# Kernel tuning notes

Measured on AMD Instinct MI355X. Metric: run time of the kernel, lower is better.

## Reference

```python
import jax, jax.numpy as jnp
import numpy as np
import math

H = 16          # n_heads
D = 1024        # hidden_dim
HD = D // H     # head_dim = 64
LR = 256        # Linformer low-rank length L
MAX_T = 4096    # max_seq_len


def setup_inputs() -> dict:
    key = jax.random.key(0)
    ks = jax.random.split(key, 7)
    X = jax.random.normal(ks[0], (4, 4096, D), dtype=jnp.float32)
    # lecun_normal ~ N(0, 1/fan_in)
    W_kernel = jax.random.normal(ks[1], (D, 3 * D), dtype=jnp.float32) / math.sqrt(D)
    W_bias = jnp.zeros((3 * D,), dtype=jnp.float32)
    low_rank_E = jax.random.normal(ks[2], (MAX_T, H, LR), dtype=jnp.float32) / math.sqrt(MAX_T)
    low_rank_V = jax.random.normal(ks[3], (MAX_T, H, LR), dtype=jnp.float32) / math.sqrt(MAX_T)
    o_kernel = jax.random.normal(ks[4], (D, D), dtype=jnp.float32) / math.sqrt(D)
    o_bias = jnp.zeros((D,), dtype=jnp.float32)
    return {"X": X, "W_kernel": W_kernel, "W_bias": W_bias,
            "low_rank_E": low_rank_E, "low_rank_V": low_rank_V,
            "o_kernel": o_kernel, "o_bias": o_bias}


def reference(X, W_kernel, W_bias, low_rank_E, low_rank_V, o_kernel, o_bias):
    B, T, _ = X.shape
    # L2-normalize tokens
    norm = jnp.linalg.norm(X, ord=2, axis=-1, keepdims=True)  # (B,T,1)
    Xn = X / norm
    # fused QKV projection
    qkv = Xn @ W_kernel + W_bias                 # (B,T,3D)
    qkv = qkv.reshape(B, T, 3, H, HD)
    Q, K, V = qkv[:, :, 0], qkv[:, :, 1], qkv[:, :, 2]   # (B,T,H,HD)
    # low-rank sequence projection of K/V: T -> L
    E = low_rank_E[:T]                            # (T,H,L)
    F = low_rank_V[:T]                            # (T,H,L)
    Kp = jnp.einsum('THK,BTHD->BHKD', E, K)       # (B,H,L,HD)
    Vp = jnp.einsum('THK,BTHD->BHKD', F, V)       # (B,H,L,HD)
    Qh = Q.transpose(0, 2, 1, 3)                  # (B,H,T,HD)
    logits = jnp.einsum('BHTD,BHKD->BHTK', Qh, Kp) / math.sqrt(HD)
    attn = jax.nn.softmax(logits, axis=-1)        # (B,H,T,L)
    out = jnp.einsum('BHTK,BHKD->BHTD', attn, Vp) # (B,H,T,HD)
    out = out.transpose(0, 2, 1, 3).reshape(B, T, H * HD)
    return out @ o_kernel + o_bias
```

## Files before the change

kernel.cpp:

```cpp
#include <hip/hip_runtime.h>
#include <stdint.h>

typedef unsigned short u16;
typedef uint32_t u32;
typedef __bf16 bf16x8 __attribute__((ext_vector_type(8)));
typedef float f32x4 __attribute__((ext_vector_type(4)));

__device__ __forceinline__ u16 f2bf(float f) {
    u32 u = __builtin_bit_cast(u32, f);
    u += 0x7fffu + ((u >> 16) & 1u);
    return (u16)(u >> 16);
}

__device__ __forceinline__ f32x4 mfma16(bf16x8 a, bf16x8 b, f32x4 c) {
    return __builtin_amdgcn_mfma_f32_16x16x32_bf16(a, b, c, 0, 0, 0);
}

__device__ __forceinline__ void gld_lds16(void* lds, const void* g) {
    __builtin_amdgcn_global_load_lds(
        (__attribute__((address_space(1))) void*)(uintptr_t)g,
        (__attribute__((address_space(3))) void*)(u32)(uintptr_t)lds,
        16, 0, 0);
}

__global__ __launch_bounds__(256) void k_norm(const float* __restrict__ X,
                                              u16* __restrict__ Xn) {
    const int row = blockIdx.x;
    const float4 v = ((const float4*)(X + (size_t)row * 1024))[threadIdx.x];
    float ss = v.x * v.x + v.y * v.y + v.z * v.z + v.w * v.w;
#pragma unroll
    for (int m = 1; m < 64; m <<= 1) ss += __shfl_xor(ss, m);
    __shared__ float red[4];
    if ((threadIdx.x & 63) == 0) red[threadIdx.x >> 6] = ss;
    __syncthreads();
    const float sc = 1.0f / sqrtf(red[0] + red[1] + red[2] + red[3]);
    ushort4 o;
    o.x = f2bf(v.x * sc); o.y = f2bf(v.y * sc);
    o.z = f2bf(v.z * sc); o.w = f2bf(v.w * sc);
    ((ushort4*)(Xn + (size_t)row * 1024))[threadIdx.x] = o;
}

__global__ __launch_bounds__(256) void k_transpose_cast64(
    const float* __restrict__ src, u16* __restrict__ dst,
    int R, int rstride, long zsrc, long zdst) {
    __shared__ float tile[64][65];
    src += (size_t)blockIdx.z * zsrc;
    dst += (size_t)blockIdx.z * zdst;
    const int c0 = blockIdx.x * 64, r0 = blockIdx.y * 64;
    const int tid = threadIdx.x;
    const int lr = tid >> 4, lc = tid & 15;
#pragma unroll
    for (int i = 0; i < 4; ++i) {
        const int r = lr + i * 16;
        const float4 v = *(const float4*)(src + (size_t)(r0 + r) * rstride + c0 + lc * 4);
        tile[r][lc * 4 + 0] = v.x; tile[r][lc * 4 + 1] = v.y;
        tile[r][lc * 4 + 2] = v.z; tile[r][lc * 4 + 3] = v.w;
    }
    __syncthreads();
    const int c = tid >> 2, seg = tid & 3;
    u32 w[8];
#pragma unroll
    for (int j = 0; j < 8; ++j) {
        const u32 lo = f2bf(tile[seg * 16 + 2 * j][c]);
        const u32 hi = f2bf(tile[seg * 16 + 2 * j + 1][c]);
        w[j] = lo | (hi << 16);
    }
    u16* dp = dst + (size_t)(c0 + c) * R + r0 + seg * 16;
    uint4 q0; q0.x = w[0]; q0.y = w[1]; q0.z = w[2]; q0.w = w[3];
    uint4 q1; q1.x = w[4]; q1.y = w[5]; q1.z = w[6]; q1.w = w[7];
    *(uint4*)dp = q0;
    *((uint4*)dp + 1) = q1;
}

#define G8_PRE(Aptr, Bptr)                                                       \
    const int tid = threadIdx.x, lane = tid & 63;                                \
    const int wid = tid >> 6, wm = wid >> 2, wn = wid & 3;                       \
    const int cl = lane & 15, g = lane >> 4;                                     \
    const int colb = (tid & 7) * 16;                                             \
    const int scb = colb ^ (((tid >> 3) & 7) << 4);                              \
    const int rbA = ((tid >> 3) & 31) + ((tid >> 8) << 7);                       \
    const int rbB = tid >> 3;                                                    \
    const char* gA = (const char*)(Aptr) + (size_t)(m0 + rbA) * 2048 + scb;      \
    const char* gB = (const char*)(Bptr) + (size_t)(n0 + rbB) * 2048 + scb;      \
    const u32 lA = (u32)(rbA * 128 + colb);                                      \
    const u32 lB = (u32)(65536 + rbB * 128 + colb);                              \
    const int xr0 = (g * 16) ^ ((cl & 7) << 4);                                  \
    const int xr1 = (64 + g * 16) ^ ((cl & 7) << 4);

#define G8_STA(q, tau, beta) gld_lds16(sm + (beta) + lA + (q) * 4096,            \
                                       gA + (q) * 65536 + (size_t)(tau) * 128);
#define G8_STB(c, tau, beta) gld_lds16(sm + (beta) + lB + (c) * 8192,            \
                                       gB + (c) * 131072 + (size_t)(tau) * 128);

#define G8_RDB(beta)                                                             \
    _Pragma("unroll") for (int nf = 0; nf < 4; ++nf) {                           \
        const u32 rb_ = (beta) + 65536 + (u32)(wn * 64 + nf * 16 + cl) * 128;    \
        bF[nf][0] = *(const bf16x8*)(sm + rb_ + xr0);                            \
        bF[nf][1] = *(const bf16x8*)(sm + rb_ + xr1);                            \
    }
#define G8_RDA(q, beta)                                                          \
    _Pragma("unroll") for (int m = 0; m < 2; ++m) {                              \
        const u32 ra_ = (beta) + (u32)(wm * 128 + (q) * 32 + m * 16 + cl) * 128; \
        aF[m][0] = *(const bf16x8*)(sm + ra_ + xr0);                             \
        aF[m][1] = *(const bf16x8*)(sm + ra_ + xr1);                             \
    }

#define G8_MMA(q)                                                                \
    asm volatile("s_waitcnt lgkmcnt(0)" ::: "memory");                           \
    __builtin_amdgcn_sched_barrier(0);                                           \
    __builtin_amdgcn_s_setprio(1);                                               \
    _Pragma("unroll") for (int m = 0; m < 2; ++m)                                \
        _Pragma("unroll") for (int nf = 0; nf < 4; ++nf) {                       \
            acc[(q)*2 + m][nf] = mfma16(aF[m][0], bF[nf][0], acc[(q)*2 + m][nf]);\
            acc[(q)*2 + m][nf] = mfma16(aF[m][1], bF[nf][1], acc[(q)*2 + m][nf]);\
        }                                                                        \
    __builtin_amdgcn_s_setprio(0);                                               \
    __builtin_amdgcn_s_barrier();                                                \
    __builtin_amdgcn_sched_barrier(0);

#define G8_LOOP                                                                  \
    bf16x8 aF[2][2], bF[4][2];                                                   \
    G8_STA(0, 0, 0) G8_STB(0, 0, 0) G8_STA(1, 0, 0) G8_STB(1, 0, 0)              \
    G8_STA(2, 0, 0) G8_STB(2, 0, 0) G8_STA(3, 0, 0) G8_STB(3, 0, 0)              \
    G8_STA(0, 1, 32768) G8_STB(0, 1, 32768)                                      \
    G8_STA(1, 1, 32768) G8_STB(1, 1, 32768)                                      \
    G8_STA(2, 1, 32768) G8_STB(2, 1, 32768)                                      \
    for (int it = 0; it < 8; ++it) {                                             \
        const int t1 = 2 * it + 1, t2v = 2 * it + 2, t3v = 2 * it + 3;           \
        const bool nt = (it < 7);                                                \
                                                                         \
        G8_STA(3, t1, 32768) G8_STB(3, t1, 32768)                                \
        asm volatile("s_waitcnt vmcnt(8)" ::: "memory");                         \
        __builtin_amdgcn_s_barrier();                                            \
        G8_RDB(0) G8_RDA(0, 0) G8_MMA(0)                                         \
                                                                         \
        if (nt) { G8_STA(0, t2v, 0) G8_STB(0, t2v, 0) }                          \
        G8_RDA(1, 0) G8_MMA(1)                                                   \
                                                                         \
        if (nt) { G8_STA(1, t2v, 0) G8_STB(1, t2v, 0) }                          \
        G8_RDA(2, 0) G8_MMA(2)                                                   \
                                                                         \
        if (nt) { G8_STA(2, t2v, 0) G8_STB(2, t2v, 0) }                          \
        G8_RDA(3, 0) G8_MMA(3)                                                   \
                                                                         \
        if (nt) {                                                                \
            G8_STA(3, t2v, 0) G8_STB(3, t2v, 0)                                  \
            asm volatile("s_waitcnt vmcnt(8)" ::: "memory");                     \
        } else {                                                                 \
            asm volatile("s_waitcnt vmcnt(0)" ::: "memory");                     \
        }                                                                        \
        __builtin_amdgcn_s_barrier();                                            \
        G8_RDB(32768) G8_RDA(0, 32768) G8_MMA(0)                                 \
                                                                         \
        if (nt) { G8_STA(0, t3v, 32768) G8_STB(0, t3v, 32768) }                  \
        G8_RDA(1, 32768) G8_MMA(1)                                               \
                                                                         \
        if (nt) { G8_STA(1, t3v, 32768) G8_STB(1, t3v, 32768) }                  \
        G8_RDA(2, 32768) G8_MMA(2)                                               \
                                                                         \
        if (nt) { G8_STA(2, t3v, 32768) G8_STB(2, t3v, 32768) }                  \
        G8_RDA(3, 32768) G8_MMA(3)                                               \
    }

__global__ __launch_bounds__(512, 2) void k_gemm_qkv(
    const u16* __restrict__ A, const u16* __restrict__ Bt,
    const float* __restrict__ bias,
    u16* __restrict__ Qo, u16* __restrict__ Kt, u16* __restrict__ Vt) {
    __shared__ __align__(16) char sm[131072];
    u32 bid = blockIdx.x;
    bid = (bid & 7) * 96 + (bid >> 3);
    const int m0 = (int)(bid / 12) * 256, n0 = (int)(bid % 12) * 256;

    G8_PRE(A, Bt)

    const f32x4 fz = {0.f, 0.f, 0.f, 0.f};
    f32x4 acc[8][4];
#pragma unroll
    for (int i = 0; i < 8; ++i)
#pragma unroll
        for (int j = 0; j < 4; ++j) acc[i][j] = fz;

    G8_LOOP

#pragma unroll
    for (int mf = 0; mf < 8; ++mf) {
        const int mbase = m0 + wm * 128 + mf * 16 + g * 4;
        const int b = mbase >> 12;
        const int t = mbase & 4095;
#pragma unroll
        for (int nf = 0; nf < 4; ++nf) {
            const int n = n0 + wn * 64 + nf * 16 + cl;
            const float bv = bias[n];
            const int seg = n >> 10;
            const int hd = n & 1023;
            f32x4 v = acc[mf][nf];
            if (seg == 0) {
#pragma unroll
                for (int r = 0; r < 4; ++r)
                    Qo[(size_t)(mbase + r) * 1024 + hd] = f2bf(v[r] + bv);
            } else {
                u16* dst = (seg == 1) ? Kt : Vt;
                ushort4 pk;
                pk.x = f2bf(v[0] + bv); pk.y = f2bf(v[1] + bv);
                pk.z = f2bf(v[2] + bv); pk.w = f2bf(v[3] + bv);
                *(ushort4*)(dst + (size_t)(b * 1024 + hd) * 4096 + t) = pk;
            }
        }
    }
}

__global__ __launch_bounds__(512, 2) void k_gemm_out(
    const u16* __restrict__ A, const u16* __restrict__ Bt,
    const float* __restrict__ bias, float* __restrict__ out) {
    __shared__ __align__(16) char sm[131072];
    u32 bid = blockIdx.x;
    bid = (bid & 7) * 32 + (bid >> 3);
    const int m0 = (int)(bid / 4) * 256, n0 = (int)(bid % 4) * 256;

    G8_PRE(A, Bt)

    const f32x4 fz = {0.f, 0.f, 0.f, 0.f};
    f32x4 acc[8][4];
#pragma unroll
    for (int i = 0; i < 8; ++i)
#pragma unroll
        for (int j = 0; j < 4; ++j) acc[i][j] = fz;

    G8_LOOP

#pragma unroll
    for (int mf = 0; mf < 8; ++mf) {
        const int mbase = m0 + wm * 128 + mf * 16 + g * 4;
#pragma unroll
        for (int nf = 0; nf < 4; ++nf) {
            const int n = n0 + wn * 64 + nf * 16 + cl;
            const float bv = bias[n];
            f32x4 v = acc[mf][nf];
#pragma unroll
            for (int r = 0; r < 4; ++r)
                out[(size_t)(mbase + r) * 1024 + n] = v[r] + bv;
        }
    }
}

__global__ __launch_bounds__(512) void k_gemm_kpvp(
    const u16* __restrict__ Et, const u16* __restrict__ Ft,
    const u16* __restrict__ Kt, const u16* __restrict__ Vt,
    float* __restrict__ Pp) {
    __shared__ __align__(16) char sm[49152];
    const int tid = threadIdx.x, lane = tid & 63, wid = tid >> 6;
    const int wm = wid >> 2, wn = wid & 3;
    const int cl = lane & 15, g = lane >> 4;
    const int mT = blockIdx.x;
    const int hs = blockIdx.y;
    const int h = hs & 15, s = hs >> 4;
    const int ks = blockIdx.z;

    const u16* Ab = (s ? Ft : Et) + (size_t)h * (256 * 4096)
                    + (size_t)(mT * 128) * 4096 + ks * 1024;
    const u16* Bb = s ? Vt : Kt;

    const int rA = tid >> 2, c16 = tid & 3;
    const int scol = (c16 ^ ((rA >> 1) & 3)) * 8;
    const u16* gA = Ab + (size_t)rA * 4096 + scol;
    const int rB1 = rA + 128;
    const u16* gB0 = Bb + (size_t)((((rA >> 6) * 16 + h) * 64) + (rA & 63)) * 4096
                     + ks * 1024 + scol;
    const u16* gB1 = Bb + (size_t)((((rB1 >> 6) * 16 + h) * 64) + (rB1 & 63)) * 4096
                     + ks * 1024 + scol;
    const u32 lA = (u32)(rA * 64 + c16 * 16);
    const u32 lB0 = (u32)(8192 + rA * 64 + c16 * 16);
    const u32 lB1 = (u32)(8192 + rB1 * 64 + c16 * 16);
    const int xsw = (g ^ ((cl >> 1) & 3)) * 16;

    const f32x4 fz = {0.f, 0.f, 0.f, 0.f};
    f32x4 acc[4][4];
#pragma unroll
    for (int i = 0; i < 4; ++i)
#pragma unroll
        for (int j = 0; j < 4; ++j) acc[i][j] = fz;

    gld_lds16(sm + lA, gA); gld_lds16(sm + lB0, gB0); gld_lds16(sm + lB1, gB1);

    u32 roff = 0;
    for (int kt = 0; kt < 32; ++kt) {
        const u32 woff = roff ^ 24576;
        if (kt < 31) {
            gld_lds16(sm + woff + lA, gA + (kt + 1) * 32);
            gld_lds16(sm + woff + lB0, gB0 + (kt + 1) * 32);
            gld_lds16(sm + woff + lB1, gB1 + (kt + 1) * 32);
            asm volatile("s_waitcnt vmcnt(3)" ::: "memory");
        } else {
            asm volatile("s_waitcnt vmcnt(0)" ::: "memory");
        }
        __builtin_amdgcn_s_barrier();
        __builtin_amdgcn_sched_barrier(0);
        const char* rb = sm + roff;
        bf16x8 aF[4], bF[4];
#pragma unroll
        for (int mf = 0; mf < 4; ++mf)
            aF[mf] = *(const bf16x8*)(rb + (wm * 64 + mf * 16 + cl) * 64 + xsw);
#pragma unroll
        for (int nf = 0; nf < 4; ++nf)
            bF[nf] = *(const bf16x8*)(rb + 8192 + (wn * 64 + nf * 16 + cl) * 64 + xsw);
        asm volatile("s_waitcnt lgkmcnt(0)" ::: "memory");
        __builtin_amdgcn_sched_barrier(0);
        __builtin_amdgcn_s_setprio(1);
#pragma unroll
        for (int mf = 0; mf < 4; ++mf)
#pragma unroll
            for (int nf = 0; nf < 4; ++nf)
                acc[mf][nf] = mfma16(aF[mf], bF[nf], acc[mf][nf]);
        __builtin_amdgcn_s_setprio(0);
        asm volatile("s_waitcnt lgkmcnt(0)" ::: "memory");
        __builtin_amdgcn_s_barrier();
        roff = woff;
    }

    float* P = Pp + ((size_t)(ks * 32 + hs) << 16);
#pragma unroll
    for (int mf = 0; mf < 4; ++mf) {
        const int m = mT * 128 + wm * 64 + mf * 16 + g * 4;
#pragma unroll
        for (int nf = 0; nf < 4; ++nf) {
            const int dcat = wn * 64 + nf * 16 + cl;
            f32x4 v = acc[mf][nf];
#pragma unroll
            for (int r = 0; r < 4; ++r)
                P[(size_t)(m + r) * 256 + dcat] = v[r];
        }
    }
}

__global__ __launch_bounds__(256) void k_red(const float* __restrict__ Pp,
                                             u16* __restrict__ Kp,
                                             u16* __restrict__ Vpt) {
    const int e = blockIdx.x * 256 + threadIdx.x;
    const int hs = e >> 14;
    const int rem = (e & 16383) * 4;
    float4 sum = {0.f, 0.f, 0.f, 0.f};
#pragma unroll
    for (int ks = 0; ks < 4; ++ks) {
        const float4 v = *(const float4*)(Pp + (((size_t)(ks * 32 + hs)) << 16) + rem);
        sum.x += v.x; sum.y += v.y; sum.z += v.z; sum.w += v.w;
    }
    const int m = rem >> 8, dcat = rem & 255;
    const int h = hs & 15, sf = hs >> 4;
    const int bh = (dcat >> 6) * 16 + h, d0 = dcat & 63;
    if (sf == 0) {
        ushort4 pk;
        pk.x = f2bf(sum.x); pk.y = f2bf(sum.y);
        pk.z = f2bf(sum.z); pk.w = f2bf(sum.w);
        *(ushort4*)(Kp + (size_t)bh * 16384 + m * 64 + d0) = pk;
    } else {
        u16* vp = Vpt + (size_t)bh * 16384 + m;
        vp[(d0 + 0) * 256] = f2bf(sum.x);
        vp[(d0 + 1) * 256] = f2bf(sum.y);
        vp[(d0 + 2) * 256] = f2bf(sum.z);
        vp[(d0 + 3) * 256] = f2bf(sum.w);
    }
}

__global__ __launch_bounds__(256, 1) void k_attn(
    const u16* __restrict__ Q, const u16* __restrict__ Kp,
    const u16* __restrict__ Vpt, u16* __restrict__ AO) {
    __shared__ __align__(16) char sm[65536];
    const int lane = threadIdx.x & 63, wid = threadIdx.x >> 6;
    const int cl = lane & 15, g = lane >> 4;
    const int tT = blockIdx.x, h = blockIdx.y, b = blockIdx.z;
    const int bh = b * 16 + h;
    const int trow0 = b * 4096 + tT * 128 + wid * 32;
    const u16* Qb = Q + (size_t)trow0 * 1024 + h * 64;
    const u16* KpB = Kp + (size_t)bh * (256 * 64);
    const u16* VpB = Vpt + (size_t)bh * (64 * 256);
    char* sP = sm + wid * 16384;

    bf16x8 qF[2][2];
#pragma unroll
    for (int nf = 0; nf < 2; ++nf)
#pragma unroll
        for (int ks = 0; ks < 2; ++ks)
            qF[nf][ks] = *(const bf16x8*)(Qb + (size_t)(nf * 16 + cl) * 1024 + ks * 32 + g * 8);

    const f32x4 fz = {0.f, 0.f, 0.f, 0.f};
    f32x4 Sp[16][2];
#pragma unroll
    for (int mf = 0; mf < 16; ++mf) { Sp[mf][0] = fz; Sp[mf][1] = fz; }

#pragma unroll
    for (int mf = 0; mf < 16; ++mf) {
#pragma unroll
        for (int ks = 0; ks < 2; ++ks) {
            bf16x8 aF = *(const bf16x8*)(KpB + (size_t)(mf * 16 + cl) * 64 + ks * 32 + g * 8);
            Sp[mf][0] = mfma16(aF, qF[0][ks], Sp[mf][0]);
            Sp[mf][1] = mfma16(aF, qF[1][ks], Sp[mf][1]);
        }
    }

    float inv_sum[2];
#pragma unroll
    for (int nf = 0; nf < 2; ++nf) {
        float mx = -1e30f;
#pragma unroll
        for (int mf = 0; mf < 16; ++mf)
#pragma unroll
            for (int r = 0; r < 4; ++r) {
                float x = Sp[mf][nf][r] * 0.125f;
                Sp[mf][nf][r] = x;
                mx = fmaxf(mx, x);
            }
        mx = fmaxf(mx, __shfl_xor(mx, 16));
        mx = fmaxf(mx, __shfl_xor(mx, 32));
        float sum = 0.f;
#pragma unroll
        for (int mf = 0; mf < 16; ++mf)
#pragma unroll
            for (int r = 0; r < 4; ++r) {
                float p = __expf(Sp[mf][nf][r] - mx);
                Sp[mf][nf][r] = p;
                sum += p;
            }
        sum += __shfl_xor(sum, 16);
        sum += __shfl_xor(sum, 32);
        inv_sum[nf] = 1.0f / sum;

        const int tl = nf * 16 + cl;
        const int sw = (tl & 7) << 4;
#pragma unroll
        for (int mf = 0; mf < 16; ++mf) {
            uint2 pk;
            pk.x = (u32)f2bf(Sp[mf][nf][0]) | ((u32)f2bf(Sp[mf][nf][1]) << 16);
            pk.y = (u32)f2bf(Sp[mf][nf][2]) | ((u32)f2bf(Sp[mf][nf][3]) << 16);
            *(uint2*)(sP + ((tl * 512 + (mf * 16 + g * 4) * 2) ^ sw)) = pk;
        }
    }

    f32x4 Oa[4][2];
#pragma unroll
    for (int mf = 0; mf < 4; ++mf) { Oa[mf][0] = fz; Oa[mf][1] = fz; }
#pragma unroll
    for (int ks = 0; ks < 8; ++ks) {
        bf16x8 aF[4];
#pragma unroll
        for (int mf = 0; mf < 4; ++mf)
            aF[mf] = *(const bf16x8*)(VpB + (size_t)(mf * 16 + cl) * 256 + ks * 32 + g * 8);
#pragma unroll
        for (int nf = 0; nf < 2; ++nf) {
            const int tl = nf * 16 + cl;
            const int sw = (tl & 7) << 4;
            bf16x8 bF = *(const bf16x8*)(sP + ((tl * 512 + (ks * 32 + g * 8) * 2) ^ sw));
#pragma unroll
            for (int mf = 0; mf < 4; ++mf)
                Oa[mf][nf] = mfma16(aF[mf], bF, Oa[mf][nf]);
        }
    }

#pragma unroll
    for (int nf = 0; nf < 2; ++nf) {
        const int t = trow0 + nf * 16 + cl;
#pragma unroll
        for (int mf = 0; mf < 4; ++mf) {
            f32x4 v = Oa[mf][nf];
            ushort4 pk;
            pk.x = f2bf(v[0] * inv_sum[nf]); pk.y = f2bf(v[1] * inv_sum[nf]);
            pk.z = f2bf(v[2] * inv_sum[nf]); pk.w = f2bf(v[3] * inv_sum[nf]);
            *(ushort4*)(AO + (size_t)t * 1024 + h * 64 + mf * 16 + g * 4) = pk;
        }
    }
}

extern "C" void kernel_launch(void* const* d_in, const int* in_sizes, int n_in,
                              void* d_out, int out_size, void* d_ws, size_t ws_size,
                              hipStream_t stream) {
    const float* X  = (const float*)d_in[0];
    const float* Wk = (const float*)d_in[1];
    const float* Wb = (const float*)d_in[2];
    const float* E  = (const float*)d_in[3];
    const float* F  = (const float*)d_in[4];
    const float* Ok = (const float*)d_in[5];
    const float* Ob = (const float*)d_in[6];
    float* out = (float*)d_out;
    char* ws = (char*)d_ws;

    u16* Xn  = (u16*)(ws + 0);
    u16* Wt  = (u16*)(ws + 33554432);
    u16* Ot  = (u16*)(ws + 39845888);
    u16* Et  = (u16*)(ws + 41943040);
    u16* Ft  = (u16*)(ws + 75497472);
    u16* Qb  = (u16*)(ws + 109051904);
    u16* Kt  = (u16*)(ws + 142606336);
    u16* Vt  = (u16*)(ws + 176160768);
    u16* Kp  = (u16*)(ws + 209715200);
    u16* Vpt = (u16*)(ws + 211812352);
    float* Pp = (float*)(ws + 0);
    u16* AO  = Xn;

    k_norm<<<16384, 256, 0, stream>>>(X, Xn);
    k_transpose_cast64<<<dim3(48, 16, 1), 256, 0, stream>>>(Wk, Wt, 1024, 3072, 0, 0);
    k_transpose_cast64<<<dim3(16, 16, 1), 256, 0, stream>>>(Ok, Ot, 1024, 1024, 0, 0);
    k_transpose_cast64<<<dim3(4, 64, 16), 256, 0, stream>>>(E, Et, 4096, 4096, 256, 1048576);
    k_transpose_cast64<<<dim3(4, 64, 16), 256, 0, stream>>>(F, Ft, 4096, 4096, 256, 1048576);
    k_gemm_qkv<<<768, 512, 0, stream>>>(Xn, Wt, Wb, Qb, Kt, Vt);
    k_gemm_kpvp<<<dim3(2, 32, 4), 512, 0, stream>>>(Et, Ft, Kt, Vt, Pp);
    k_red<<<2048, 256, 0, stream>>>(Pp, Kp, Vpt);
    k_attn<<<dim3(32, 16, 4), 256, 0, stream>>>(Qb, Kp, Vpt, AO);
    k_gemm_out<<<256, 512, 0, stream>>>(AO, Ot, Ob, out);
}
```

Measured before the change: 375.3 us.

## Double-buffer A fragments in QKV GEMM and swap operands for V projection

In the QKV GEMM main loop, A fragments now alternate between two register sets, so the LDS reads for the next quarter are issued before the MFMAs of the current one. Each wait becomes a partial lgkmcnt(4) instead of a full drain, which overlaps LDS latency with matrix math. In the low-rank projection kernel, the V path swaps the A and B operands so the result comes out already transposed. The reduction kernel can then write Vpt with one packed 8-byte store instead of four scattered 2-byte stores. The cost is more VGPRs for the extra fragment buffer, which could hurt occupancy at the launch bound of 2 blocks.

```diff
diff --git a/kernel.cpp b/kernel.cpp
--- a/kernel.cpp
+++ b/kernel.cpp
@@ -98,28 +98,31 @@
         bF[nf][0] = *(const bf16x8*)(sm + rb_ + xr0);                            \
         bF[nf][1] = *(const bf16x8*)(sm + rb_ + xr1);                            \
     }
-#define G8_RDA(q, beta)                                                          \
+#define G8_RDA2(dst, q, beta)                                                    \
     _Pragma("unroll") for (int m = 0; m < 2; ++m) {                              \
         const u32 ra_ = (beta) + (u32)(wm * 128 + (q) * 32 + m * 16 + cl) * 128; \
-        aF[m][0] = *(const bf16x8*)(sm + ra_ + xr0);                             \
-        aF[m][1] = *(const bf16x8*)(sm + ra_ + xr1);                             \
-    }
-
-#define G8_MMA(q)                                                                \
-    asm volatile("s_waitcnt lgkmcnt(0)" ::: "memory");                           \
-    __builtin_amdgcn_sched_barrier(0);                                           \
+        dst[m][0] = *(const bf16x8*)(sm + ra_ + xr0);                            \
+        dst[m][1] = *(const bf16x8*)(sm + ra_ + xr1);                            \
+    }
+
+#define G8_WAIT4 asm volatile("s_waitcnt lgkmcnt(4)" ::: "memory");              \
+    __builtin_amdgcn_sched_barrier(0);
+#define G8_WAIT0 asm volatile("s_waitcnt lgkmcnt(0)" ::: "memory");              \
+    __builtin_amdgcn_sched_barrier(0);
+
+#define G8_MMA(q, SRC)                                                           \
     __builtin_amdgcn_s_setprio(1);                                               \
     _Pragma("unroll") for (int m = 0; m < 2; ++m)                                \
         _Pragma("unroll") for (int nf = 0; nf < 4; ++nf) {                       \
-            acc[(q)*2 + m][nf] = mfma16(aF[m][0], bF[nf][0], acc[(q)*2 + m][nf]);\
-            acc[(q)*2 + m][nf] = mfma16(aF[m][1], bF[nf][1], acc[(q)*2 + m][nf]);\
+            acc[(q)*2 + m][nf] = mfma16(SRC[m][0], bF[nf][0], acc[(q)*2 + m][nf]);\
+            acc[(q)*2 + m][nf] = mfma16(SRC[m][1], bF[nf][1], acc[(q)*2 + m][nf]);\
         }                                                                        \
     __builtin_amdgcn_s_setprio(0);                                               \
     __builtin_amdgcn_s_barrier();                                                \
     __builtin_amdgcn_sched_barrier(0);
 
 #define G8_LOOP                                                                  \
-    bf16x8 aF[2][2], bF[4][2];                                                   \
+    bf16x8 aFe[2][2], aFo[2][2], bF[4][2];                                       \
     G8_STA(0, 0, 0) G8_STB(0, 0, 0) G8_STA(1, 0, 0) G8_STB(1, 0, 0)              \
     G8_STA(2, 0, 0) G8_STB(2, 0, 0) G8_STA(3, 0, 0) G8_STB(3, 0, 0)              \
     G8_STA(0, 1, 32768) G8_STB(0, 1, 32768)                                      \
@@ -132,16 +135,19 @@
         G8_STA(3, t1, 32768) G8_STB(3, t1, 32768)                                \
         asm volatile("s_waitcnt vmcnt(8)" ::: "memory");                         \
         __builtin_amdgcn_s_barrier();                                            \
-        G8_RDB(0) G8_RDA(0, 0) G8_MMA(0)                                         \
+        G8_RDB(0) G8_RDA2(aFe, 0, 0) G8_RDA2(aFo, 1, 0)                          \
+        G8_WAIT4 G8_MMA(0, aFe)                                                  \
                                                                          \
         if (nt) { G8_STA(0, t2v, 0) G8_STB(0, t2v, 0) }                          \
-        G8_RDA(1, 0) G8_MMA(1)                                                   \
+        G8_RDA2(aFe, 2, 0)                                                       \
+        G8_WAIT4 G8_MMA(1, aFo)                                                  \
                                                                          \
         if (nt) { G8_STA(1, t2v, 0) G8_STB(1, t2v, 0) }                          \
-        G8_RDA(2, 0) G8_MMA(2)                                                   \
+        G8_RDA2(aFo, 3, 0)                                                       \
+        G8_WAIT4 G8_MMA(2, aFe)                                                  \
                                                                          \
         if (nt) { G8_STA(2, t2v, 0) G8_STB(2, t2v, 0) }                          \
-        G8_RDA(3, 0) G8_MMA(3)                                                   \
+        G8_WAIT0 G8_MMA(3, aFo)                                                  \
                                                                          \
         if (nt) {                                                                \
             G8_STA(3, t2v, 0) G8_STB(3, t2v, 0)                                  \
@@ -150,16 +156,19 @@
             asm volatile("s_waitcnt vmcnt(0)" ::: "memory");                     \
         }                                                                        \
         __builtin_amdgcn_s_barrier();                                            \
-        G8_RDB(32768) G8_RDA(0, 32768) G8_MMA(0)                                 \
+        G8_RDB(32768) G8_RDA2(aFe, 0, 32768) G8_RDA2(aFo, 1, 32768)              \
+        G8_WAIT4 G8_MMA(0, aFe)                                                  \
                                                                          \
         if (nt) { G8_STA(0, t3v, 32768) G8_STB(0, t3v, 32768) }                  \
-        G8_RDA(1, 32768) G8_MMA(1)                                               \
+        G8_RDA2(aFe, 2, 32768)                                                   \
+        G8_WAIT4 G8_MMA(1, aFo)                                                  \
                                                                          \
         if (nt) { G8_STA(1, t3v, 32768) G8_STB(1, t3v, 32768) }                  \
-        G8_RDA(2, 32768) G8_MMA(2)                                               \
+        G8_RDA2(aFo, 3, 32768)                                                   \
+        G8_WAIT4 G8_MMA(2, aFe)                                                  \
                                                                          \
         if (nt) { G8_STA(2, t3v, 32768) G8_STB(2, t3v, 32768) }                  \
-        G8_RDA(3, 32768) G8_MMA(3)                                               \
+        G8_WAIT0 G8_MMA(3, aFo)                                                  \
     }
 
 __global__ __launch_bounds__(512, 2) void k_gemm_qkv(
@@ -256,21 +265,27 @@
     const int h = hs & 15, s = hs >> 4;
     const int ks = blockIdx.z;
 
-    const u16* Ab = (s ? Ft : Et) + (size_t)h * (256 * 4096)
-                    + (size_t)(mT * 128) * 4096 + ks * 1024;
-    const u16* Bb = s ? Vt : Kt;
-
     const int rA = tid >> 2, c16 = tid & 3;
     const int scol = (c16 ^ ((rA >> 1) & 3)) * 8;
-    const u16* gA = Ab + (size_t)rA * 4096 + scol;
-    const int rB1 = rA + 128;
-    const u16* gB0 = Bb + (size_t)((((rA >> 6) * 16 + h) * 64) + (rA & 63)) * 4096
-                     + ks * 1024 + scol;
-    const u16* gB1 = Bb + (size_t)((((rB1 >> 6) * 16 + h) * 64) + (rB1 & 63)) * 4096
-                     + ks * 1024 + scol;
+    const u16 *gA, *gB0, *gB1;
+    if (s == 0) {
+        gA = Et + (size_t)h * (256 * 4096) + (size_t)(mT * 128 + rA) * 4096
+             + ks * 1024 + scol;
+        gB0 = Kt + (size_t)((((rA >> 6) * 16 + h) * 64) + (rA & 63)) * 4096
+              + ks * 1024 + scol;
+        const int rB1 = rA + 128;
+        gB1 = Kt + (size_t)((((rB1 >> 6) * 16 + h) * 64) + (rB1 & 63)) * 4096
+              + ks * 1024 + scol;
+    } else {
+        const int dc = mT * 128 + rA;
+        gA = Vt + (size_t)(((dc >> 6) * 16 + h) * 64 + (dc & 63)) * 4096
+             + ks * 1024 + scol;
+        gB0 = Ft + (size_t)h * (256 * 4096) + (size_t)rA * 4096 + ks * 1024 + scol;
+        gB1 = gB0 + (size_t)128 * 4096;
+    }
     const u32 lA = (u32)(rA * 64 + c16 * 16);
     const u32 lB0 = (u32)(8192 + rA * 64 + c16 * 16);
-    const u32 lB1 = (u32)(8192 + rB1 * 64 + c16 * 16);
+    const u32 lB1 = lB0 + 128 * 64;
     const int xsw = (g ^ ((cl >> 1) & 3)) * 16;
 
     const f32x4 fz = {0.f, 0.f, 0.f, 0.f};
@@ -323,11 +338,11 @@
         const int m = mT * 128 + wm * 64 + mf * 16 + g * 4;
 #pragma unroll
         for (int nf = 0; nf < 4; ++nf) {
-            const int dcat = wn * 64 + nf * 16 + cl;
+            const int nn = wn * 64 + nf * 16 + cl;
             f32x4 v = acc[mf][nf];
 #pragma unroll
             for (int r = 0; r < 4; ++r)
-                P[(size_t)(m + r) * 256 + dcat] = v[r];
+                P[(size_t)(m + r) * 256 + nn] = v[r];
         }
     }
 }
@@ -344,20 +359,17 @@
         const float4 v = *(const float4*)(Pp + (((size_t)(ks * 32 + hs)) << 16) + rem);
         sum.x += v.x; sum.y += v.y; sum.z += v.z; sum.w += v.w;
     }
-    const int m = rem >> 8, dcat = rem & 255;
+    const int m = rem >> 8, col = rem & 255;
     const int h = hs & 15, sf = hs >> 4;
-    const int bh = (dcat >> 6) * 16 + h, d0 = dcat & 63;
+    ushort4 pk;
+    pk.x = f2bf(sum.x); pk.y = f2bf(sum.y);
+    pk.z = f2bf(sum.z); pk.w = f2bf(sum.w);
     if (sf == 0) {
-        ushort4 pk;
-        pk.x = f2bf(sum.x); pk.y = f2bf(sum.y);
-        pk.z = f2bf(sum.z); pk.w = f2bf(sum.w);
+        const int bh = (col >> 6) * 16 + h, d0 = col & 63;
         *(ushort4*)(Kp + (size_t)bh * 16384 + m * 64 + d0) = pk;
     } else {
-        u16* vp = Vpt + (size_t)bh * 16384 + m;
-        vp[(d0 + 0) * 256] = f2bf(sum.x);
-        vp[(d0 + 1) * 256] = f2bf(sum.y);
-        vp[(d0 + 2) * 256] = f2bf(sum.z);
-        vp[(d0 + 3) * 256] = f2bf(sum.w);
+        const int bh = (m >> 6) * 16 + h, d = m & 63;
+        *(ushort4*)(Vpt + (size_t)bh * 16384 + d * 256 + col) = pk;
     }
 }
 
```

After: 365.6 us. -2.6%, faster.
